# Performance work log

Hardware: AMD Instinct MI355X
Metric: run time of the kernel (lower is better)

## Reference

```python
import jax, jax.numpy as jnp
import numpy as np

N_QUBITS = 4
N_LAYERS = 2
FS = 2          # filter_size
STRIDE = 1
DIM = 2 ** N_QUBITS  # 16

# mean over qubits of PauliZ eigenvalue per computational-basis state
_idx = np.arange(DIM)
_bits = np.stack([(_idx >> (N_QUBITS - 1 - q)) & 1 for q in range(N_QUBITS)], 0)  # [4,16]
Z_MEAN = jnp.asarray((1.0 - 2.0 * _bits).mean(0), dtype=jnp.float32)               # [16]


def ry_mat(t):
    c, s = jnp.cos(t / 2), jnp.sin(t / 2)
    m = jnp.stack([jnp.stack([c, -s], -1), jnp.stack([s, c], -1)], -2)
    return m.astype(jnp.complex64)


def rx_mat(t):
    c = jnp.cos(t / 2).astype(jnp.complex64)
    s = (jnp.sin(t / 2) * (-1j)).astype(jnp.complex64)
    return jnp.stack([jnp.stack([c, s], -1), jnp.stack([s, c], -1)], -2)


def rz_mat(t):
    e = jnp.exp((t / 2).astype(jnp.complex64) * (-1j))
    z = jnp.zeros_like(e)
    return jnp.stack([jnp.stack([e, z], -1), jnp.stack([z, jnp.conj(e)], -1)], -2)


def apply_1q(state, U, q):
    # state: [N,2,2,2,2] complex; U: [2,2] or batched [N,2,2]
    st = jnp.moveaxis(state, 1 + q, -1)
    if U.ndim == 3:
        st = jnp.einsum('nab,n...b->n...a', U, st)
    else:
        st = jnp.einsum('ab,n...b->n...a', U, st)
    return jnp.moveaxis(st, -1, 1 + q)


def apply_cnot(state, c, t):
    st = jnp.moveaxis(state, (1 + c, 1 + t), (-2, -1))
    st = jnp.stack([st[..., 0, :], st[..., 1, ::-1]], axis=-2)
    return jnp.moveaxis(st, (-2, -1), (1 + c, 1 + t))


def apply_cry(state, theta, c, t):
    U = ry_mat(theta)
    st = jnp.moveaxis(state, (1 + c, 1 + t), (-2, -1))
    bot = jnp.einsum('ab,n...b->n...a', U, st[..., 1, :])
    st = jnp.stack([st[..., 0, :], bot], axis=-2)
    return jnp.moveaxis(st, (-2, -1), (1 + c, 1 + t))


def _forward(x, weights):
    B, H, W, C = x.shape
    oh = (H - FS) // STRIDE + 1
    ow = (W - FS) // STRIDE + 1
    # extract all patches at once: [B, oh, ow, FS, FS, C]
    ri = (jnp.arange(oh) * STRIDE)[:, None, None, None] + jnp.arange(FS)[None, None, :, None]
    ci = (jnp.arange(ow) * STRIDE)[None, :, None, None] + jnp.arange(FS)[None, None, None, :]
    patches = x[:, ri, ci, :]
    pf = patches.reshape(B * oh * ow, FS * FS * C)
    # tf.nn.l2_normalize over the whole (flat) patch, eps=1e-12
    norm = pf * jax.lax.rsqrt(jnp.maximum(jnp.sum(pf * pf, -1, keepdims=True), 1e-12))
    ang = norm[:, :N_QUBITS]  # RY angles, [N,4]
    N = pf.shape[0]

    # |0000> encoded state, batched over all patches
    state = jnp.zeros((N, DIM), jnp.complex64).at[:, 0].set(1.0)
    state = state.reshape((N,) + (2,) * N_QUBITS)
    for q in range(N_QUBITS):
        state = apply_1q(state, ry_mat(ang[:, q]), q)
    for q in range(N_QUBITS - 1):
        state = apply_cnot(state, q, q + 1)

    outs = []
    for f in range(weights.shape[0]):
        w = weights[f]
        s = state
        for layer in range(N_LAYERS):
            base = layer * N_QUBITS * 3
            for q in range(N_QUBITS):
                p = base + q * 3
                s = apply_1q(s, rx_mat(w[p]), q)
                s = apply_1q(s, ry_mat(w[p + 1]), q)
                s = apply_1q(s, rz_mat(w[p + 2]), q)
            # CRY on even pairs, reusing weights[base + i] (as in the source)
            for q in range(0, N_QUBITS - 1, 2):
                s = apply_cry(s, w[base + q], q, q + 1)
        sf = s.reshape(N, DIM)
        probs = jnp.real(sf * jnp.conj(sf))           # [N,16]
        outs.append((probs @ Z_MEAN).reshape(B, oh, ow))  # mean of <Z_q>
    return jnp.stack(outs, -1)  # [B, oh, ow, n_filters]


def setup_inputs() -> dict:
    key = jax.random.key(0)
    k1, k2 = jax.random.split(key)
    x = jax.random.normal(k1, (8, 96, 96, 16), dtype=jnp.float32)
    # keras 'random_uniform' initializer default range
    weights = jax.random.uniform(k2, (8, 24), dtype=jnp.float32, minval=-0.05, maxval=0.05)
    return {"x": x, "weights": weights}


def reference(x, weights):
    return _forward(x, weights)
```

## Files before the change

### kernel.cpp

```cpp
#include <hip/hip_runtime.h>

namespace {
constexpr int DIM = 16;
constexpr int BATCH = 8;
constexpr int H = 96, W = 96, CH = 16;
constexpr int OH = 95, OW = 95;
constexpr int NF = 8, NW = 24;
constexpr int NPIX = BATCH * OH * OW;
constexpr int PSIBLK = (NPIX + 255) / 256;
constexpr int M_FLOATS = NF * 256;
constexpr int PSI_OFF = M_FLOATS;
constexpr int PPB = 32;
constexpr int APBLK = (NPIX + PPB - 1) / PPB;
constexpr int MPAD = 260;
}

__device__ __forceinline__ int permf(int i) {
  int j = i;
  if (j & 8) j ^= 4;
  if (j & 4) j ^= 2;
  if (j & 2) j ^= 1;
  return j;
}

__global__ __launch_bounds__(256)
void prep_kernel(const float* __restrict__ x, const float* __restrict__ wts,
                 float* __restrict__ ws) {
  const int tid = threadIdx.x;
  if (blockIdx.x == PSIBLK) {
    __shared__ float ur[NF * 256];
    __shared__ float ui[NF * 256];
    const int f = tid >> 4;
    const int col = tid & 15;
    if (tid < NF * DIM) {
      const float* w = wts + f * NW;
      float ar[DIM], ai[DIM];
#pragma unroll
      for (int i = 0; i < DIM; ++i) { ar[i] = (i == col) ? 1.f : 0.f; ai[i] = 0.f; }
#pragma unroll
      for (int layer = 0; layer < 2; ++layer) {
        const int wb = layer * 12;
#pragma unroll
        for (int q = 0; q < 4; ++q) {
          const int m = 8 >> q;
          float c, s;
          {
            __sincosf(w[wb + q * 3] * 0.5f, &s, &c);
#pragma unroll
            for (int i = 0; i < DIM; ++i) {
              if (i & m) continue;
              const int j = i | m;
              const float a0r = ar[i], a0i = ai[i], a1r = ar[j], a1i = ai[j];
              ar[i] = fmaf(c, a0r,  s * a1i);
              ai[i] = fmaf(c, a0i, -s * a1r);
              ar[j] = fmaf(c, a1r,  s * a0i);
              ai[j] = fmaf(c, a1i, -s * a0r);
            }
          }
          {
            __sincosf(w[wb + q * 3 + 1] * 0.5f, &s, &c);
#pragma unroll
            for (int i = 0; i < DIM; ++i) {
              if (i & m) continue;
              const int j = i | m;
              const float a0r = ar[i], a0i = ai[i], a1r = ar[j], a1i = ai[j];
              ar[i] = fmaf(c, a0r, -s * a1r);
              ai[i] = fmaf(c, a0i, -s * a1i);
              ar[j] = fmaf(s, a0r,  c * a1r);
              ai[j] = fmaf(s, a0i,  c * a1i);
            }
          }
          {
            __sincosf(w[wb + q * 3 + 2] * 0.5f, &s, &c);
#pragma unroll
            for (int i = 0; i < DIM; ++i) {
              const float r = ar[i], im = ai[i];
              if (i & m) { ar[i] = fmaf(c, r, -s * im); ai[i] = fmaf(c, im,  s * r); }
              else       { ar[i] = fmaf(c, r,  s * im); ai[i] = fmaf(c, im, -s * r); }
            }
          }
        }
        {
          float c, s;
          __sincosf(w[wb + 0] * 0.5f, &s, &c);
#pragma unroll
          for (int i = 0; i < DIM; ++i) {
            if (!(i & 8) || (i & 4)) continue;
            const int j = i | 4;
            const float a0r = ar[i], a0i = ai[i], a1r = ar[j], a1i = ai[j];
            ar[i] = fmaf(c, a0r, -s * a1r);
            ai[i] = fmaf(c, a0i, -s * a1i);
            ar[j] = fmaf(s, a0r,  c * a1r);
            ai[j] = fmaf(s, a0i,  c * a1i);
          }
        }
        {
          float c, s;
          __sincosf(w[wb + 2] * 0.5f, &s, &c);
#pragma unroll
          for (int i = 0; i < DIM; ++i) {
            if (!(i & 2) || (i & 1)) continue;
            const int j = i | 1;
            const float a0r = ar[i], a0i = ai[i], a1r = ar[j], a1i = ai[j];
            ar[i] = fmaf(c, a0r, -s * a1r);
            ai[i] = fmaf(c, a0i, -s * a1i);
            ar[j] = fmaf(s, a0r,  c * a1r);
            ai[j] = fmaf(s, a0i,  c * a1i);
          }
        }
      }
#pragma unroll
      for (int i = 0; i < DIM; ++i) {
        ur[f * 256 + col * 16 + i] = ar[i];
        ui[f * 256 + col * 16 + i] = ai[i];
      }
    }
    __syncthreads();
    if (tid < NF * DIM) {
      const int k = col;
      const int pk = permf(k);
      const float* cr = ur + f * 256;
      const float* ci = ui + f * 256;
      float* dst = ws + f * 256 + k * 16;
#pragma unroll
      for (int j = 0; j < DIM; ++j) {
        const int pj = permf(j);
        float acc = 0.f;
#pragma unroll
        for (int i = 0; i < DIM; ++i) {
          const float z = 1.f - 0.5f * (float)__popc(i);
          acc += z * (cr[pk * 16 + i] * cr[pj * 16 + i] +
                      ci[pk * 16 + i] * ci[pj * 16 + i]);
        }
        dst[j] = acc;
      }
    }
  } else {
    const int n = blockIdx.x * 256 + tid;
    if (n >= NPIX) return;
    const int b = n / (OH * OW);
    const int rem = n - b * (OH * OW);
    const int oi = rem / OW;
    const int oj = rem - oi * OW;

    const float* base = x + (((b * H) + oi) * W + oj) * CH;
    float ss = 0.f;
    float4 f0 = make_float4(0.f, 0.f, 0.f, 0.f);
#pragma unroll
    for (int fi = 0; fi < 2; ++fi) {
      const float4* row = reinterpret_cast<const float4*>(base + fi * W * CH);
#pragma unroll
      for (int k = 0; k < 8; ++k) {
        const float4 v = row[k];
        if (fi == 0 && k == 0) f0 = v;
        ss = fmaf(v.x, v.x, ss); ss = fmaf(v.y, v.y, ss);
        ss = fmaf(v.z, v.z, ss); ss = fmaf(v.w, v.w, ss);
      }
    }
    const float inv = rsqrtf(fmaxf(ss, 1e-12f));

    float cq[4], sq[4];
    __sincosf(f0.x * inv * 0.5f, &sq[0], &cq[0]);
    __sincosf(f0.y * inv * 0.5f, &sq[1], &cq[1]);
    __sincosf(f0.z * inv * 0.5f, &sq[2], &cq[2]);
    __sincosf(f0.w * inv * 0.5f, &sq[3], &cq[3]);

    float st[DIM];
#pragma unroll
    for (int i = 0; i < DIM; ++i) {
      st[i] = ((i & 8) ? sq[0] : cq[0]) * ((i & 4) ? sq[1] : cq[1]) *
              ((i & 2) ? sq[2] : cq[2]) * ((i & 1) ? sq[3] : cq[3]);
    }
    float4* dst = reinterpret_cast<float4*>(ws + PSI_OFF + n * 16);
    dst[0] = make_float4(st[0], st[1], st[2], st[3]);
    dst[1] = make_float4(st[4], st[5], st[6], st[7]);
    dst[2] = make_float4(st[8], st[9], st[10], st[11]);
    dst[3] = make_float4(st[12], st[13], st[14], st[15]);
  }
}

__global__ __launch_bounds__(256)
void apply_kernel(const float* __restrict__ ws, float* __restrict__ out) {
  __shared__ float M[NF * MPAD];
  const int tid = threadIdx.x;
#pragma unroll
  for (int it = 0; it < 2; ++it) {
    const int i = it * 256 + tid;
    const int ff = i >> 6;
    const int r = i & 63;
    reinterpret_cast<float4*>(M + ff * MPAD)[r] =
        reinterpret_cast<const float4*>(ws)[i];
  }
  __syncthreads();

  const int p = tid >> 3;
  const int f = tid & 7;
  const int n = blockIdx.x * PPB + p;
  const bool valid = n < NPIX;
  const int nc = valid ? n : NPIX - 1;

  float psi[DIM];
  {
    const float4* pp = reinterpret_cast<const float4*>(ws + PSI_OFF + nc * 16);
    const float4 a0 = pp[0], a1 = pp[1], a2 = pp[2], a3 = pp[3];
    psi[0] = a0.x;  psi[1] = a0.y;  psi[2] = a0.z;  psi[3] = a0.w;
    psi[4] = a1.x;  psi[5] = a1.y;  psi[6] = a1.z;  psi[7] = a1.w;
    psi[8] = a2.x;  psi[9] = a2.y;  psi[10] = a2.z; psi[11] = a2.w;
    psi[12] = a3.x; psi[13] = a3.y; psi[14] = a3.z; psi[15] = a3.w;
  }

  float yv[DIM];
#pragma unroll
  for (int i = 0; i < DIM; ++i) yv[i] = 0.f;

  const float4* mrow = reinterpret_cast<const float4*>(M + f * MPAD);
#pragma unroll
  for (int k = 0; k < DIM; ++k) {
    const float t = psi[k];
    const float4 m0 = mrow[k * 4 + 0];
    const float4 m1 = mrow[k * 4 + 1];
    const float4 m2 = mrow[k * 4 + 2];
    const float4 m3 = mrow[k * 4 + 3];
    yv[0]  = fmaf(m0.x, t, yv[0]);  yv[1]  = fmaf(m0.y, t, yv[1]);
    yv[2]  = fmaf(m0.z, t, yv[2]);  yv[3]  = fmaf(m0.w, t, yv[3]);
    yv[4]  = fmaf(m1.x, t, yv[4]);  yv[5]  = fmaf(m1.y, t, yv[5]);
    yv[6]  = fmaf(m1.z, t, yv[6]);  yv[7]  = fmaf(m1.w, t, yv[7]);
    yv[8]  = fmaf(m2.x, t, yv[8]);  yv[9]  = fmaf(m2.y, t, yv[9]);
    yv[10] = fmaf(m2.z, t, yv[10]); yv[11] = fmaf(m2.w, t, yv[11]);
    yv[12] = fmaf(m3.x, t, yv[12]); yv[13] = fmaf(m3.y, t, yv[13]);
    yv[14] = fmaf(m3.z, t, yv[14]); yv[15] = fmaf(m3.w, t, yv[15]);
  }

  float s0 = 0.f, s1 = 0.f, s2 = 0.f, s3 = 0.f;
#pragma unroll
  for (int i = 0; i < DIM; i += 4) {
    s0 = fmaf(psi[i + 0], yv[i + 0], s0);
    s1 = fmaf(psi[i + 1], yv[i + 1], s1);
    s2 = fmaf(psi[i + 2], yv[i + 2], s2);
    s3 = fmaf(psi[i + 3], yv[i + 3], s3);
  }
  if (valid) out[blockIdx.x * 256 + tid] = (s0 + s1) + (s2 + s3);
}

extern "C" void kernel_launch(void* const* d_in, const int* in_sizes, int n_in,
                              void* d_out, int out_size, void* d_ws, size_t ws_size,
                              hipStream_t stream) {
  const float* x = (const float*)d_in[0];
  const float* w = (const float*)d_in[1];
  float* out = (float*)d_out;
  float* ws = (float*)d_ws;

  prep_kernel<<<dim3(PSIBLK + 1), dim3(256), 0, stream>>>(x, w, ws);
  apply_kernel<<<dim3(APBLK), dim3(256), 0, stream>>>(ws, out);
}
```

Measured before the change: 78.03 us.

## Map filters to wavefronts with uniform scalar M loads and two pixels per lane

```diff
diff --git a/kernel.cpp b/kernel.cpp
--- a/kernel.cpp
+++ b/kernel.cpp
@@ -8,11 +8,9 @@
 constexpr int NF = 8, NW = 24;
 constexpr int NPIX = BATCH * OH * OW;
 constexpr int PSIBLK = (NPIX + 255) / 256;
-constexpr int M_FLOATS = NF * 256;
-constexpr int PSI_OFF = M_FLOATS;
-constexpr int PPB = 32;
-constexpr int APBLK = (NPIX + PPB - 1) / PPB;
-constexpr int MPAD = 260;
+constexpr int PSI_OFF = NF * 256;
+constexpr int PPB = 128;
+constexpr int ABLK = (NPIX + PPB - 1) / PPB;
 }
 
 __device__ __forceinline__ int permf(int i) {
@@ -179,67 +177,78 @@
   }
 }
 
-__global__ __launch_bounds__(256)
+__global__ __launch_bounds__(512)
 void apply_kernel(const float* __restrict__ ws, float* __restrict__ out) {
-  __shared__ float M[NF * MPAD];
+  __shared__ float os[PPB * 9];
   const int tid = threadIdx.x;
-#pragma unroll
-  for (int it = 0; it < 2; ++it) {
-    const int i = it * 256 + tid;
-    const int ff = i >> 6;
-    const int r = i & 63;
-    reinterpret_cast<float4*>(M + ff * MPAD)[r] =
-        reinterpret_cast<const float4*>(ws)[i];
-  }
+  const int lane = tid & 63;
+  const int f = __builtin_amdgcn_readfirstlane(tid >> 6);
+  const float* __restrict__ M = ws + f * 256;
+  const int pbase = blockIdx.x * PPB;
+
+  const int n0 = pbase + lane;
+  const int n1 = pbase + 64 + lane;
+  const int c0 = n0 < NPIX ? n0 : NPIX - 1;
+  const int c1 = n1 < NPIX ? n1 : NPIX - 1;
+
+  float pa[DIM], pb[DIM];
+  {
+    const float4* p0 = reinterpret_cast<const float4*>(ws + PSI_OFF + c0 * 16);
+    const float4 a0 = p0[0], a1 = p0[1], a2 = p0[2], a3 = p0[3];
+    pa[0] = a0.x;  pa[1] = a0.y;  pa[2] = a0.z;  pa[3] = a0.w;
+    pa[4] = a1.x;  pa[5] = a1.y;  pa[6] = a1.z;  pa[7] = a1.w;
+    pa[8] = a2.x;  pa[9] = a2.y;  pa[10] = a2.z; pa[11] = a2.w;
+    pa[12] = a3.x; pa[13] = a3.y; pa[14] = a3.z; pa[15] = a3.w;
+    const float4* p1 = reinterpret_cast<const float4*>(ws + PSI_OFF + c1 * 16);
+    const float4 b0 = p1[0], b1 = p1[1], b2 = p1[2], b3 = p1[3];
+    pb[0] = b0.x;  pb[1] = b0.y;  pb[2] = b0.z;  pb[3] = b0.w;
+    pb[4] = b1.x;  pb[5] = b1.y;  pb[6] = b1.z;  pb[7] = b1.w;
+    pb[8] = b2.x;  pb[9] = b2.y;  pb[10] = b2.z; pb[11] = b2.w;
+    pb[12] = b3.x; pb[13] = b3.y; pb[14] = b3.z; pb[15] = b3.w;
+  }
+
+  float ya[DIM], yb[DIM];
+#pragma unroll
+  for (int i = 0; i < DIM; ++i) { ya[i] = 0.f; yb[i] = 0.f; }
+
+#pragma unroll
+  for (int k = 0; k < DIM; ++k) {
+    const float ak = pa[k];
+    const float bk = pb[k];
+#pragma unroll
+    for (int j = 0; j < DIM; ++j) {
+      const float m = M[k * 16 + j];
+      ya[j] = fmaf(m, ak, ya[j]);
+      yb[j] = fmaf(m, bk, yb[j]);
+    }
+  }
+
+  float a0 = 0.f, a1 = 0.f, a2 = 0.f, a3 = 0.f;
+  float b0 = 0.f, b1 = 0.f, b2 = 0.f, b3 = 0.f;
+#pragma unroll
+  for (int i = 0; i < DIM; i += 4) {
+    a0 = fmaf(pa[i + 0], ya[i + 0], a0);
+    a1 = fmaf(pa[i + 1], ya[i + 1], a1);
+    a2 = fmaf(pa[i + 2], ya[i + 2], a2);
+    a3 = fmaf(pa[i + 3], ya[i + 3], a3);
+    b0 = fmaf(pb[i + 0], yb[i + 0], b0);
+    b1 = fmaf(pb[i + 1], yb[i + 1], b1);
+    b2 = fmaf(pb[i + 2], yb[i + 2], b2);
+    b3 = fmaf(pb[i + 3], yb[i + 3], b3);
+  }
+  os[lane * 9 + f] = (a0 + a1) + (a2 + a3);
+  os[(64 + lane) * 9 + f] = (b0 + b1) + (b2 + b3);
   __syncthreads();
 
-  const int p = tid >> 3;
-  const int f = tid & 7;
-  const int n = blockIdx.x * PPB + p;
-  const bool valid = n < NPIX;
-  const int nc = valid ? n : NPIX - 1;
-
-  float psi[DIM];
-  {
-    const float4* pp = reinterpret_cast<const float4*>(ws + PSI_OFF + nc * 16);
-    const float4 a0 = pp[0], a1 = pp[1], a2 = pp[2], a3 = pp[3];
-    psi[0] = a0.x;  psi[1] = a0.y;  psi[2] = a0.z;  psi[3] = a0.w;
-    psi[4] = a1.x;  psi[5] = a1.y;  psi[6] = a1.z;  psi[7] = a1.w;
-    psi[8] = a2.x;  psi[9] = a2.y;  psi[10] = a2.z; psi[11] = a2.w;
-    psi[12] = a3.x; psi[13] = a3.y; psi[14] = a3.z; psi[15] = a3.w;
-  }
-
-  float yv[DIM];
-#pragma unroll
-  for (int i = 0; i < DIM; ++i) yv[i] = 0.f;
-
-  const float4* mrow = reinterpret_cast<const float4*>(M + f * MPAD);
-#pragma unroll
-  for (int k = 0; k < DIM; ++k) {
-    const float t = psi[k];
-    const float4 m0 = mrow[k * 4 + 0];
-    const float4 m1 = mrow[k * 4 + 1];
-    const float4 m2 = mrow[k * 4 + 2];
-    const float4 m3 = mrow[k * 4 + 3];
-    yv[0]  = fmaf(m0.x, t, yv[0]);  yv[1]  = fmaf(m0.y, t, yv[1]);
-    yv[2]  = fmaf(m0.z, t, yv[2]);  yv[3]  = fmaf(m0.w, t, yv[3]);
-    yv[4]  = fmaf(m1.x, t, yv[4]);  yv[5]  = fmaf(m1.y, t, yv[5]);
-    yv[6]  = fmaf(m1.z, t, yv[6]);  yv[7]  = fmaf(m1.w, t, yv[7]);
-    yv[8]  = fmaf(m2.x, t, yv[8]);  yv[9]  = fmaf(m2.y, t, yv[9]);
-    yv[10] = fmaf(m2.z, t, yv[10]); yv[11] = fmaf(m2.w, t, yv[11]);
-    yv[12] = fmaf(m3.x, t, yv[12]); yv[13] = fmaf(m3.y, t, yv[13]);
-    yv[14] = fmaf(m3.z, t, yv[14]); yv[15] = fmaf(m3.w, t, yv[15]);
-  }
-
-  float s0 = 0.f, s1 = 0.f, s2 = 0.f, s3 = 0.f;
-#pragma unroll
-  for (int i = 0; i < DIM; i += 4) {
-    s0 = fmaf(psi[i + 0], yv[i + 0], s0);
-    s1 = fmaf(psi[i + 1], yv[i + 1], s1);
-    s2 = fmaf(psi[i + 2], yv[i + 2], s2);
-    s3 = fmaf(psi[i + 3], yv[i + 3], s3);
-  }
-  if (valid) out[blockIdx.x * 256 + tid] = (s0 + s1) + (s2 + s3);
+  const int j2 = tid * 2;
+  const int p = j2 >> 3;
+  const int e = j2 & 7;
+  const long gi = (long)pbase * 8 + j2;
+  if (gi + 1 < (long)NPIX * 8) {
+    const float v0 = os[p * 9 + e];
+    const float v1 = os[p * 9 + e + 1];
+    *reinterpret_cast<float2*>(out + gi) = make_float2(v0, v1);
+  }
 }
 
 extern "C" void kernel_launch(void* const* d_in, const int* in_sizes, int n_in,
@@ -251,5 +260,5 @@
   float* ws = (float*)d_ws;
 
   prep_kernel<<<dim3(PSIBLK + 1), dim3(256), 0, stream>>>(x, w, ws);
-  apply_kernel<<<dim3(APBLK), dim3(256), 0, stream>>>(ws, out);
-}
+  apply_kernel<<<dim3(ABLK), dim3(512), 0, stream>>>(ws, out);
+}
```

New measurement: 76.60 us. About the same (-1.8%).
